# Optimization experiments

Measured on AMD Instinct MI355X. Metric: run time of the kernel, lower is better.

## Reference

```python
import jax, jax.numpy as jnp
import numpy as np

NEG_INF = -1e15  # matches masked_fill value -1000000000000000.0
ALPHA = 0.2      # leakyReLU negative slope


def setup_inputs() -> dict:
    key = jax.random.key(0)
    k1, k2, k3, k4 = jax.random.split(key, 4)
    N, F_IN, F_OUT = 8192, 256, 64
    x = jax.random.normal(k1, (N, F_IN), dtype=jnp.float32)
    mask = jax.random.randint(k2, (N, N), 0, 2, dtype=jnp.int32)
    trans = jax.random.normal(k3, (F_IN, F_OUT), dtype=jnp.float32) * 0.1
    attn = jax.random.normal(k4, (2 * F_OUT, 1), dtype=jnp.float32) * 0.1
    return {"x": x, "mask": mask, "trans": trans, "attn": attn}


def reference(x, mask, trans, attn):
    d = trans.shape[1]
    h = x @ trans                                  # [N, d]
    e1 = h @ attn[:d, :]                           # [N, 1]
    e2 = h @ attn[d:, :]                           # [N, 1]
    scores = jax.nn.leaky_relu(e1 + e2.T, negative_slope=ALPHA)  # [N, N]
    masked = jnp.where(mask == 0, NEG_INF, scores)
    attention = jax.nn.softmax(masked, axis=1)
    return attention @ h                           # [N, d]
```

## Files before the change

### kernel.cpp

```cpp
#include <hip/hip_runtime.h>
#include <hip/hip_bf16.h>
#include <math.h>

#define N 8192
#define FIN 256
#define D 64
#define ALPHA 0.2f

typedef __attribute__((ext_vector_type(8))) short bf16x8;
typedef __attribute__((ext_vector_type(4))) float f32x4;

__global__ __launch_bounds__(256) void k_h_e(
    const float* __restrict__ x, const float* __restrict__ trans,
    const float* __restrict__ attn,
    __hip_bfloat16* __restrict__ hT, float* __restrict__ e1, float* __restrict__ e2)
{
    __shared__ float xT[FIN * 34];
    __shared__ __hip_bfloat16 hl[32 * D];
    const int t = threadIdx.x;
    const int r0 = blockIdx.x * 32;

    #pragma unroll
    for (int v = 0; v < 8; ++v) {
        int fidx = v * 256 + t;
        int r = fidx & 31, c4 = fidx >> 5;
        float4 xv = *(const float4*)(x + (size_t)(r0 + r) * FIN + c4 * 4);
        xT[(c4 * 4 + 0) * 34 + r] = xv.x;
        xT[(c4 * 4 + 1) * 34 + r] = xv.y;
        xT[(c4 * 4 + 2) * 34 + r] = xv.z;
        xT[(c4 * 4 + 3) * 34 + r] = xv.w;
    }
    __syncthreads();

    const int cg = t & 15, g = t >> 4;
    const int d0 = cg * 4;
    const float4 a1 = *(const float4*)(attn + d0);
    const float4 a2 = *(const float4*)(attn + D + d0);

    float acc0[4] = {0.f, 0.f, 0.f, 0.f};
    float acc1[4] = {0.f, 0.f, 0.f, 0.f};
    #pragma unroll 4
    for (int k = 0; k < FIN; ++k) {
        const float2 xp = *(const float2*)(xT + k * 34 + 2 * g);
        const float4 tv = *(const float4*)(trans + k * D + d0);
        acc0[0] = fmaf(xp.x, tv.x, acc0[0]);
        acc0[1] = fmaf(xp.x, tv.y, acc0[1]);
        acc0[2] = fmaf(xp.x, tv.z, acc0[2]);
        acc0[3] = fmaf(xp.x, tv.w, acc0[3]);
        acc1[0] = fmaf(xp.y, tv.x, acc1[0]);
        acc1[1] = fmaf(xp.y, tv.y, acc1[1]);
        acc1[2] = fmaf(xp.y, tv.z, acc1[2]);
        acc1[3] = fmaf(xp.y, tv.w, acc1[3]);
    }
    const int row0 = r0 + 2 * g, row1 = row0 + 1;

    float p1a = acc0[0]*a1.x + acc0[1]*a1.y + acc0[2]*a1.z + acc0[3]*a1.w;
    float p1b = acc1[0]*a1.x + acc1[1]*a1.y + acc1[2]*a1.z + acc1[3]*a1.w;
    float p2a = acc0[0]*a2.x + acc0[1]*a2.y + acc0[2]*a2.z + acc0[3]*a2.w;
    float p2b = acc1[0]*a2.x + acc1[1]*a2.y + acc1[2]*a2.z + acc1[3]*a2.w;
    #pragma unroll
    for (int m君 = 1; m君 <= 8; m君 <<= 1) {
        p1a += __shfl_xor(p1a, m君);
        p1b += __shfl_xor(p1b, m君);
        p2a += __shfl_xor(p2a, m君);
        p2b += __shfl_xor(p2b, m君);
    }
    if (cg == 0) {
        e1[row0] = p1a; e1[row1] = p1b;
        e2[row0] = p2a; e2[row1] = p2b;
    }

    __hip_bfloat162* hp0 = (__hip_bfloat162*)(hl + (2 * g) * D + d0);
    __hip_bfloat162* hp1 = (__hip_bfloat162*)(hl + (2 * g + 1) * D + d0);
    hp0[0] = __float22bfloat162_rn(make_float2(acc0[0], acc0[1]));
    hp0[1] = __float22bfloat162_rn(make_float2(acc0[2], acc0[3]));
    hp1[0] = __float22bfloat162_rn(make_float2(acc1[0], acc1[1]));
    hp1[1] = __float22bfloat162_rn(make_float2(acc1[2], acc1[3]));
    __syncthreads();
    {
        const int d = t >> 2, rs = (t & 3) * 8;
        union { bf16x8 v; __hip_bfloat16 h[8]; } o;
        #pragma unroll
        for (int i = 0; i < 8; ++i) o.h[i] = hl[(rs + i) * D + d];
        *(bf16x8*)(hT + (size_t)d * N + r0 + rs) = o.v;
    }
}

__global__ __launch_bounds__(256) void k_attn(
    const int* __restrict__ mask, const __hip_bfloat16* __restrict__ hT,
    const float* __restrict__ e1, const float* __restrict__ e2,
    float* __restrict__ acc_part, float* __restrict__ l_part, int cs)
{
    const int t = threadIdx.x;
    const int lane = t & 63, wave = t >> 6;
    const int i0 = (blockIdx.y * 4 + wave) * 16;
    const int sp = blockIdx.x;
    const int c0 = sp * cs;
    const int m = lane & 15, quad = lane >> 4;
    const int row = i0 + m;
    const float er = e1[row];
    const size_t mrow = (size_t)row * N;

    f32x4 acc0 = {0.f, 0.f, 0.f, 0.f};
    f32x4 acc1 = {0.f, 0.f, 0.f, 0.f};
    f32x4 acc2 = {0.f, 0.f, 0.f, 0.f};
    f32x4 acc3 = {0.f, 0.f, 0.f, 0.f};
    float lsum = 0.f;

    const __hip_bfloat16* hb0 = hT + (size_t)(m     ) * N;
    const __hip_bfloat16* hb1 = hT + (size_t)(m + 16) * N;
    const __hip_bfloat16* hb2 = hT + (size_t)(m + 32) * N;
    const __hip_bfloat16* hb3 = hT + (size_t)(m + 48) * N;

    for (int j = c0; j < c0 + cs; j += 32) {
        const int jb = j + quad * 8;
        const int4   m0 = *(const int4*)(mask + mrow + jb);
        const int4   m1 = *(const int4*)(mask + mrow + jb + 4);
        const float4 ea = *(const float4*)(e2 + jb);
        const float4 eb = *(const float4*)(e2 + jb + 4);
        const bf16x8 b0 = *(const bf16x8*)(hb0 + jb);
        const bf16x8 b1 = *(const bf16x8*)(hb1 + jb);
        const bf16x8 b2 = *(const bf16x8*)(hb2 + jb);
        const bf16x8 b3 = *(const bf16x8*)(hb3 + jb);

        float s0 = er + ea.x; s0 = s0 > 0.f ? s0 : ALPHA * s0;
        float s1 = er + ea.y; s1 = s1 > 0.f ? s1 : ALPHA * s1;
        float s2 = er + ea.z; s2 = s2 > 0.f ? s2 : ALPHA * s2;
        float s3 = er + ea.w; s3 = s3 > 0.f ? s3 : ALPHA * s3;
        float s4 = er + eb.x; s4 = s4 > 0.f ? s4 : ALPHA * s4;
        float s5 = er + eb.y; s5 = s5 > 0.f ? s5 : ALPHA * s5;
        float s6 = er + eb.z; s6 = s6 > 0.f ? s6 : ALPHA * s6;
        float s7 = er + eb.w; s7 = s7 > 0.f ? s7 : ALPHA * s7;
        const float p0 = m0.x ? __expf(s0) : 0.f;
        const float p1 = m0.y ? __expf(s1) : 0.f;
        const float p2 = m0.z ? __expf(s2) : 0.f;
        const float p3 = m0.w ? __expf(s3) : 0.f;
        const float p4 = m1.x ? __expf(s4) : 0.f;
        const float p5 = m1.y ? __expf(s5) : 0.f;
        const float p6 = m1.z ? __expf(s6) : 0.f;
        const float p7 = m1.w ? __expf(s7) : 0.f;

        union { bf16x8 v; __hip_bfloat162 h2[4]; } af;
        af.h2[0] = __float22bfloat162_rn(make_float2(p0, p1));
        af.h2[1] = __float22bfloat162_rn(make_float2(p2, p3));
        af.h2[2] = __float22bfloat162_rn(make_float2(p4, p5));
        af.h2[3] = __float22bfloat162_rn(make_float2(p6, p7));

        lsum += ((p0 + p1) + (p2 + p3)) + ((p4 + p5) + (p6 + p7));

        acc0 = __builtin_amdgcn_mfma_f32_16x16x32_bf16(af.v, b0, acc0, 0, 0, 0);
        acc1 = __builtin_amdgcn_mfma_f32_16x16x32_bf16(af.v, b1, acc1, 0, 0, 0);
        acc2 = __builtin_amdgcn_mfma_f32_16x16x32_bf16(af.v, b2, acc2, 0, 0, 0);
        acc3 = __builtin_amdgcn_mfma_f32_16x16x32_bf16(af.v, b3, acc3, 0, 0, 0);
    }

    lsum += __shfl_xor(lsum, 16);
    lsum += __shfl_xor(lsum, 32);
    if (quad == 0) l_part[(size_t)sp * N + row] = lsum;

    #pragma unroll
    for (int reg = 0; reg < 4; ++reg) {
        const size_t rbase = ((size_t)sp * N + i0 + quad * 4 + reg) * D;
        acc_part[rbase + m     ] = acc0[reg];
        acc_part[rbase + m + 16] = acc1[reg];
        acc_part[rbase + m + 32] = acc2[reg];
        acc_part[rbase + m + 48] = acc3[reg];
    }
}

__global__ __launch_bounds__(256) void k_reduce(
    const float* __restrict__ acc_part, const float* __restrict__ l_part,
    float* __restrict__ out, int nsplit)
{
    const int idx = blockIdx.x * 256 + threadIdx.x;
    const int row = idx >> 6;
    float sum = 0.f, l = 0.f;
    for (int s = 0; s < nsplit; ++s) {
        sum += acc_part[(size_t)s * N * D + idx];
        l   += l_part[(size_t)s * N + row];
    }
    out[idx] = sum / l;
}

extern "C" void kernel_launch(void* const* d_in, const int* in_sizes, int n_in,
                              void* d_out, int out_size, void* d_ws, size_t ws_size,
                              hipStream_t stream) {
    const float* x     = (const float*)d_in[0];
    const int*   mask  = (const int*)d_in[1];
    const float* trans = (const float*)d_in[2];
    const float* attn  = (const float*)d_in[3];
    float* out = (float*)d_out;

    char* ws = (char*)d_ws;
    __hip_bfloat16* hT = (__hip_bfloat16*)ws;
    float* e1 = (float*)(ws + (size_t)D * N * sizeof(__hip_bfloat16));
    float* e2 = e1 + N;
    float* l_part = e2 + N;

    const size_t base = (size_t)D * N * sizeof(__hip_bfloat16)
                      + 2 * (size_t)N * sizeof(float);
    int nsplit = 1;
    const int cands[5] = {16, 8, 4, 2, 1};
    for (int ci = 0; ci < 5; ++ci) {
        int s = cands[ci];
        size_t need = base + (size_t)s * N * sizeof(float)
                    + (size_t)s * N * D * sizeof(float);
        if (need <= ws_size) { nsplit = s; break; }
    }
    float* acc_part = l_part + (size_t)nsplit * N;

    k_h_e<<<N / 32, 256, 0, stream>>>(x, trans, attn, hT, e1, e2);
    dim3 g2(nsplit, N / 64);
    k_attn<<<g2, 256, 0, stream>>>(mask, hT, e1, e2, acc_part, l_part, N / nsplit);
    k_reduce<<<(N * D) / 256, 256, 0, stream>>>(acc_part, l_part, out, nsplit);
}
```

Measured before the change: 444.5 us.

## Shrink h-projection blocks to 8 rows, unroll attention loop, cap split at 8

The projection kernel now handles 8 rows per block with one output column per lane, and it launches 4x more blocks. It loads x straight into shared memory without a transpose and reduces the e1/e2 dot products across the full wave. The attention inner loop gets an unroll-by-2 hint to expose more memory-level parallelism, and the maximum column split drops from 16 to 8, which halves the partial-sum traffic in the reduce. Each block now rereads trans from global memory more often in total, and the smaller split reduces the grid size of the dominant attention kernel.

```diff
diff --git a/kernel.cpp b/kernel.cpp
--- a/kernel.cpp
+++ b/kernel.cpp
@@ -15,74 +15,50 @@
     const float* __restrict__ attn,
     __hip_bfloat16* __restrict__ hT, float* __restrict__ e1, float* __restrict__ e2)
 {
-    __shared__ float xT[FIN * 34];
-    __shared__ __hip_bfloat16 hl[32 * D];
+    __shared__ float xs[8 * FIN];
+    __shared__ __hip_bfloat16 hl[8 * D];
     const int t = threadIdx.x;
-    const int r0 = blockIdx.x * 32;
+    const int r0 = blockIdx.x * 8;
 
     #pragma unroll
-    for (int v = 0; v < 8; ++v) {
-        int fidx = v * 256 + t;
-        int r = fidx & 31, c4 = fidx >> 5;
-        float4 xv = *(const float4*)(x + (size_t)(r0 + r) * FIN + c4 * 4);
-        xT[(c4 * 4 + 0) * 34 + r] = xv.x;
-        xT[(c4 * 4 + 1) * 34 + r] = xv.y;
-        xT[(c4 * 4 + 2) * 34 + r] = xv.z;
-        xT[(c4 * 4 + 3) * 34 + r] = xv.w;
+    for (int v = 0; v < 2; ++v) {
+        int idx = t + 256 * v;
+        ((float4*)xs)[idx] = ((const float4*)(x + (size_t)r0 * FIN))[idx];
     }
     __syncthreads();
 
-    const int cg = t & 15, g = t >> 4;
-    const int d0 = cg * 4;
-    const float4 a1 = *(const float4*)(attn + d0);
-    const float4 a2 = *(const float4*)(attn + D + d0);
+    const int lane = t & 63, w = t >> 6;
+    const float* xa = xs + (2 * w) * FIN;
+    const float* xb = xs + (2 * w + 1) * FIN;
+    float acca = 0.f, accb = 0.f;
+    #pragma unroll 8
+    for (int k = 0; k < FIN; ++k) {
+        const float tv = trans[k * D + lane];
+        acca = fmaf(xa[k], tv, acca);
+        accb = fmaf(xb[k], tv, accb);
+    }
+    const int ra = r0 + 2 * w, rb = ra + 1;
 
-    float acc0[4] = {0.f, 0.f, 0.f, 0.f};
-    float acc1[4] = {0.f, 0.f, 0.f, 0.f};
-    #pragma unroll 4
-    for (int k = 0; k < FIN; ++k) {
-        const float2 xp = *(const float2*)(xT + k * 34 + 2 * g);
-        const float4 tv = *(const float4*)(trans + k * D + d0);
-        acc0[0] = fmaf(xp.x, tv.x, acc0[0]);
-        acc0[1] = fmaf(xp.x, tv.y, acc0[1]);
-        acc0[2] = fmaf(xp.x, tv.z, acc0[2]);
-        acc0[3] = fmaf(xp.x, tv.w, acc0[3]);
-        acc1[0] = fmaf(xp.y, tv.x, acc1[0]);
-        acc1[1] = fmaf(xp.y, tv.y, acc1[1]);
-        acc1[2] = fmaf(xp.y, tv.z, acc1[2]);
-        acc1[3] = fmaf(xp.y, tv.w, acc1[3]);
+    const float a1 = attn[lane], a2 = attn[D + lane];
+    float p1a = acca * a1, p2a = acca * a2;
+    float p1b = accb * a1, p2b = accb * a2;
+    #pragma unroll
+    for (int mm = 1; mm <= 32; mm <<= 1) {
+        p1a += __shfl_xor(p1a, mm);
+        p2a += __shfl_xor(p2a, mm);
+        p1b += __shfl_xor(p1b, mm);
+        p2b += __shfl_xor(p2b, mm);
     }
-    const int row0 = r0 + 2 * g, row1 = row0 + 1;
+    if (lane == 0) { e1[ra] = p1a; e2[ra] = p2a; e1[rb] = p1b; e2[rb] = p2b; }
 
-    float p1a = acc0[0]*a1.x + acc0[1]*a1.y + acc0[2]*a1.z + acc0[3]*a1.w;
-    float p1b = acc1[0]*a1.x + acc1[1]*a1.y + acc1[2]*a1.z + acc1[3]*a1.w;
-    float p2a = acc0[0]*a2.x + acc0[1]*a2.y + acc0[2]*a2.z + acc0[3]*a2.w;
-    float p2b = acc1[0]*a2.x + acc1[1]*a2.y + acc1[2]*a2.z + acc1[3]*a2.w;
-    #pragma unroll
-    for (int m君 = 1; m君 <= 8; m君 <<= 1) {
-        p1a += __shfl_xor(p1a, m君);
-        p1b += __shfl_xor(p1b, m君);
-        p2a += __shfl_xor(p2a, m君);
-        p2b += __shfl_xor(p2b, m君);
-    }
-    if (cg == 0) {
-        e1[row0] = p1a; e1[row1] = p1b;
-        e2[row0] = p2a; e2[row1] = p2b;
-    }
-
-    __hip_bfloat162* hp0 = (__hip_bfloat162*)(hl + (2 * g) * D + d0);
-    __hip_bfloat162* hp1 = (__hip_bfloat162*)(hl + (2 * g + 1) * D + d0);
-    hp0[0] = __float22bfloat162_rn(make_float2(acc0[0], acc0[1]));
-    hp0[1] = __float22bfloat162_rn(make_float2(acc0[2], acc0[3]));
-    hp1[0] = __float22bfloat162_rn(make_float2(acc1[0], acc1[1]));
-    hp1[1] = __float22bfloat162_rn(make_float2(acc1[2], acc1[3]));
+    hl[(2 * w) * D + lane]     = __float2bfloat16(acca);
+    hl[(2 * w + 1) * D + lane] = __float2bfloat16(accb);
     __syncthreads();
-    {
-        const int d = t >> 2, rs = (t & 3) * 8;
+    if (t < D) {
         union { bf16x8 v; __hip_bfloat16 h[8]; } o;
         #pragma unroll
-        for (int i = 0; i < 8; ++i) o.h[i] = hl[(rs + i) * D + d];
-        *(bf16x8*)(hT + (size_t)d * N + r0 + rs) = o.v;
+        for (int r = 0; r < 8; ++r) o.h[r] = hl[r * D + t];
+        *(bf16x8*)(hT + (size_t)t * N + r0) = o.v;
     }
 }
 
@@ -112,6 +88,7 @@
     const __hip_bfloat16* hb2 = hT + (size_t)(m + 32) * N;
     const __hip_bfloat16* hb3 = hT + (size_t)(m + 48) * N;
 
+    #pragma unroll 2
     for (int j = c0; j < c0 + cs; j += 32) {
         const int jb = j + quad * 8;
         const int4   m0 = *(const int4*)(mask + mrow + jb);
@@ -200,8 +177,8 @@
     const size_t base = (size_t)D * N * sizeof(__hip_bfloat16)
                       + 2 * (size_t)N * sizeof(float);
     int nsplit = 1;
-    const int cands[5] = {16, 8, 4, 2, 1};
-    for (int ci = 0; ci < 5; ++ci) {
+    const int cands[4] = {8, 4, 2, 1};
+    for (int ci = 0; ci < 4; ++ci) {
         int s = cands[ci];
         size_t need = base + (size_t)s * N * sizeof(float)
                     + (size_t)s * N * D * sizeof(float);
@@ -209,7 +186,7 @@
     }
     float* acc_part = l_part + (size_t)nsplit * N;
 
-    k_h_e<<<N / 32, 256, 0, stream>>>(x, trans, attn, hT, e1, e2);
+    k_h_e<<<N / 8, 256, 0, stream>>>(x, trans, attn, hT, e1, e2);
     dim3 g2(nsplit, N / 64);
     k_attn<<<g2, 256, 0, stream>>>(mask, hT, e1, e2, acc_part, l_part, N / nsplit);
     k_reduce<<<(N * D) / 256, 256, 0, stream>>>(acc_part, l_part, out, nsplit);
```

Measured after the change: 437.6 us. About the same (-1.5%).
